# Kernel tuning notes

Measured on AMD Instinct MI355X. Metric: run time of the kernel, lower is better.

Reference implementation:

```python
import jax, jax.numpy as jnp
import numpy as np

EMBED_DIM = 768
NUM_HEADS = 12
HEAD_DIM = EMBED_DIM // NUM_HEADS

def setup_inputs() -> dict:
    key = jax.random.key(0)
    ks = jax.random.split(key, 5)
    B, N = 16, 1024
    s_qkv = 1.0 / np.sqrt(EMBED_DIM)
    s_proj = 1.0 / np.sqrt(EMBED_DIM)
    return {
        "x": jax.random.normal(ks[0], (B, N, EMBED_DIM), dtype=jnp.float32),
        "w_qkv": jax.random.uniform(ks[1], (EMBED_DIM, 3 * EMBED_DIM), jnp.float32, -s_qkv, s_qkv),
        "b_qkv": jax.random.uniform(ks[2], (3 * EMBED_DIM,), jnp.float32, -s_qkv, s_qkv),
        "w_proj": jax.random.uniform(ks[3], (EMBED_DIM, EMBED_DIM), jnp.float32, -s_proj, s_proj),
        "b_proj": jax.random.uniform(ks[4], (EMBED_DIM,), jnp.float32, -s_proj, s_proj),
    }

def reference(x, w_qkv, b_qkv, w_proj, b_proj):
    B, N, E = x.shape
    H, D = NUM_HEADS, HEAD_DIM
    qkv = x @ w_qkv + b_qkv                       # [B, N, 3E]
    qkv = qkv.reshape(B, N, 3, H, D)
    q, k, v = jnp.moveaxis(qkv, 2, 0)             # each [B, N, H, D]
    q = jnp.swapaxes(q, 1, 2)                      # [B, H, N, D]
    k = jnp.swapaxes(k, 1, 2)
    v = jnp.swapaxes(v, 1, 2)
    attn = jnp.einsum('bhnd,bhmd->bhnm', q, k) * (D ** -0.5)
    attn = jax.nn.softmax(attn, axis=-1)
    out = jnp.einsum('bhnm,bhmd->bhnd', attn, v)   # [B, H, N, D]
    out = jnp.swapaxes(out, 1, 2).reshape(B, N, E)
    return out @ w_proj + b_proj
```

## Files before the change

### kernel.cpp

```cpp
#include <hip/hip_runtime.h>
#include <hip/hip_bf16.h>


#define EDIM 768
#define NH 12
#define HD 64
#define BB 16
#define SN 1024
#define MTOT (BB*SN)

typedef __attribute__((ext_vector_type(8))) short short8;
typedef __attribute__((ext_vector_type(4))) short short4v;
typedef __attribute__((ext_vector_type(4))) float f32x4;
typedef unsigned short bfr;

#if defined(__HIP_DEVICE_COMPILE__)
#if !__has_builtin(__builtin_amdgcn_mfma_f32_16x16x16bf16_1k)
#error "missing __builtin_amdgcn_mfma_f32_16x16x16bf16_1k on device"
#endif
#endif

#define MFMA32(A,B,C) __builtin_amdgcn_mfma_f32_16x16x32_bf16(A,B,C,0,0,0)
#define MFMA16(A,B,C) __builtin_amdgcn_mfma_f32_16x16x16bf16_1k(A,B,C,0,0,0)

__device__ __forceinline__ bfr f2bf(float f) {
    union { float f; unsigned int u; } v; v.f = f;
    unsigned int u = v.u;
    u += 0x7FFFu + ((u >> 16) & 1u);
    return (bfr)(u >> 16);
}
__device__ __forceinline__ bfr f2bf_fast(float f) {
    union { float f; unsigned int u; } v; v.f = f;
    return (bfr)((v.u + 0x8000u) >> 16);
}

__device__ __forceinline__ void gl2lds16(const bfr* g, bfr* l) {
    __builtin_amdgcn_global_load_lds(
        (__attribute__((address_space(1))) void*)(g),
        (__attribute__((address_space(3))) void*)(l), 16, 0, 0);
}

__global__ void k_convert(const float* __restrict__ in, bfr* __restrict__ out, int n4) {
    const int j = (blockIdx.x & 7) * 1536 + (blockIdx.x >> 3);
    int i = j * blockDim.x + threadIdx.x;
    if (i >= n4) return;
    float4 v = ((const float4*)in)[i];
    ushort4 o;
    o.x = f2bf(v.x); o.y = f2bf(v.y); o.z = f2bf(v.z); o.w = f2bf(v.w);
    ((ushort4*)out)[i] = o;
}

__global__ void k_transpose_bf16(const float* __restrict__ in, bfr* __restrict__ out,
                                 int R, int C) {
    __shared__ float tile[32][33];
    int c0 = blockIdx.x * 32, r0 = blockIdx.y * 32;
    int tx = threadIdx.x & 31, ty = threadIdx.x >> 5;
    #pragma unroll
    for (int i = 0; i < 32; i += 8)
        tile[ty + i][tx] = in[(size_t)(r0 + ty + i) * C + c0 + tx];
    __syncthreads();
    #pragma unroll
    for (int i = 0; i < 32; i += 8)
        out[(size_t)(c0 + ty + i) * R + r0 + tx] = f2bf(tile[tx][ty + i]);
}

#define QSCALE 0.18033688011112042f
template <int EPI>
__launch_bounds__(256, 3)
__global__ void k_gemm_bt(const bfr* __restrict__ A, const bfr* __restrict__ BT,
                          const float* __restrict__ bias, float* __restrict__ out,
                          bfr* __restrict__ qb, bfr* __restrict__ kb, bfr* __restrict__ vT) {
    __shared__ bfr As[2][128 * 32];
    __shared__ bfr Bs[2][128 * 32];

    const int wgid = blockIdx.y * gridDim.x + blockIdx.x;
    const int xcd = wgid & 7;
    const int idx = wgid >> 3;
    const int half = gridDim.x << 3;
    const int band = idx / half;
    const int r = idx - band * half;
    const int n0 = (r >> 3) * 128;
    const int m0 = (xcd * 16 + band * 8 + (r & 7)) * 128;

    const int t = threadIdx.x;
    const int lane = t & 63;
    const int wave = t >> 6;
    const int wr = wave >> 1, wc = wave & 1;
    const int l15 = lane & 15, quad = lane >> 4;

    f32x4 acc[4][4] = {};

    const int srow = t >> 2;
    const int sg = ((t & 3) - (t >> 3)) & 3;
    const bfr* gA0 = A  + (size_t)(m0 + srow) * 768 + sg * 8;
    const bfr* gA1 = A  + (size_t)(m0 + 64 + srow) * 768 + sg * 8;
    const bfr* gB0 = BT + (size_t)(n0 + srow) * 768 + sg * 8;
    const bfr* gB1 = BT + (size_t)(n0 + 64 + srow) * 768 + sg * 8;
    const int w512 = wave * 512;

    const int pg = ((quad + (l15 >> 1)) & 3) * 8;

    for (int kt = 0; kt < 768; kt += 64) {
        __syncthreads();
        #pragma unroll
        for (int kh = 0; kh < 2; kh++) {
            const int ko = kt + kh * 32;
            gl2lds16(gA0 + ko, &As[kh][w512]);
            gl2lds16(gA1 + ko, &As[kh][2048 + w512]);
            gl2lds16(gB0 + ko, &Bs[kh][w512]);
            gl2lds16(gB1 + ko, &Bs[kh][2048 + w512]);
        }
        __syncthreads();

        #pragma unroll
        for (int kh = 0; kh < 2; kh++) {
            short8 af[4], bf[4];
            #pragma unroll
            for (int rt = 0; rt < 4; rt++)
                af[rt] = *(const short8*)(&As[kh][(wr * 64 + rt * 16 + l15) * 32 + pg]);
            #pragma unroll
            for (int ct = 0; ct < 4; ct++)
                bf[ct] = *(const short8*)(&Bs[kh][(wc * 64 + ct * 16 + l15) * 32 + pg]);
            #pragma unroll
            for (int rt = 0; rt < 4; rt++)
                #pragma unroll
                for (int ct = 0; ct < 4; ct++)
                    acc[rt][ct] = MFMA32(af[rt], bf[ct], acc[rt][ct]);
        }
    }

    #pragma unroll
    for (int rt = 0; rt < 4; rt++) {
        #pragma unroll
        for (int ct = 0; ct < 4; ct++) {
            const int col = n0 + wc * 64 + ct * 16 + l15;
            const float bv = bias[col];
            #pragma unroll
            for (int reg = 0; reg < 4; reg++) {
                const int m = m0 + wr * 64 + rt * 16 + quad * 4 + reg;
                float val = acc[rt][ct][reg] + bv;
                if constexpr (EPI == 0) {
                    out[(size_t)m * EDIM + col] = val;
                } else {
                    const int three = col / 768;
                    const int rem = col - three * 768;
                    const int h = rem >> 6, d = rem & 63;
                    const int b = m >> 10, n = m & 1023;
                    const size_t bh = (size_t)b * NH + h;
                    if (three == 0)      qb[(bh * SN + n) * HD + d] = f2bf(val * QSCALE);
                    else if (three == 1) kb[(bh * SN + n) * HD + d] = f2bf(val);
                    else                 vT[(bh * HD + d) * SN + n] = f2bf(val);
                }
            }
        }
    }
}

#define LDK 72

__launch_bounds__(256, 2)
__global__ void k_attn(const bfr* __restrict__ qb, const bfr* __restrict__ kb,
                       const bfr* __restrict__ vT, bfr* __restrict__ ao) {
    __shared__ bfr Ks[2][64 * LDK];
    __shared__ bfr Vs[2][64 * LDK];

    const int linear = blockIdx.y * gridDim.x + blockIdx.x;
    const int idx = linear >> 3;
    const int bh = (linear & 7) * 24 + idx % 24;
    const int q0 = (idx / 24) * 128;

    const int t = threadIdx.x;
    const int lane = t & 63, w = t >> 6;
    const int l15 = lane & 15, quad = lane >> 4;

    const bfr* qbase = qb + (size_t)bh * SN * HD;
    const bfr* kbase = kb + (size_t)bh * SN * HD;
    const bfr* vbase = vT + (size_t)bh * HD * SN;

    short8 qf[2][2];
    #pragma unroll
    for (int qt = 0; qt < 2; qt++)
        #pragma unroll
        for (int c = 0; c < 2; c++)
            qf[qt][c] = *(const short8*)(qbase + (size_t)(q0 + w * 32 + qt * 16 + l15) * HD + c * 32 + quad * 8);

    f32x4 o_acc[2][4] = {};
    f32x4 l_acc[2] = {};
    short4v ones4;
    #pragma unroll
    for (int i = 0; i < 4; i++) ones4[i] = (short)0x3F80;

    const int srow = t >> 2;
    const int scol = (t & 3) * 16;
    const bfr* gK = kbase + (size_t)srow * HD + scol;
    const bfr* gV = vbase + (size_t)srow * SN + scol;
    const int soff = srow * LDK + scol;

    uint4 kr0, kr1, vr0, vr1;
    kr0 = *(const uint4*)(gK);      kr1 = *(const uint4*)(gK + 8);
    vr0 = *(const uint4*)(gV);      vr1 = *(const uint4*)(gV + 8);
    *(uint4*)(&Ks[0][soff]) = kr0;  *(uint4*)(&Ks[0][soff + 8]) = kr1;
    *(uint4*)(&Vs[0][soff]) = vr0;  *(uint4*)(&Vs[0][soff + 8]) = vr1;

    for (int it = 0; it < SN / 64; it++) {
        const int cur = it & 1;
        const int kv0n = (it + 1) * 64;
        if (kv0n < SN) {
            kr0 = *(const uint4*)(gK + (size_t)kv0n * HD);
            kr1 = *(const uint4*)(gK + (size_t)kv0n * HD + 8);
            vr0 = *(const uint4*)(gV + kv0n);
            vr1 = *(const uint4*)(gV + kv0n + 8);
        }
        __syncthreads();
        if (kv0n < SN) {
            *(uint4*)(&Ks[cur ^ 1][soff]) = kr0;  *(uint4*)(&Ks[cur ^ 1][soff + 8]) = kr1;
            *(uint4*)(&Vs[cur ^ 1][soff]) = vr0;  *(uint4*)(&Vs[cur ^ 1][soff + 8]) = vr1;
        }

        const bfr* Kc = &Ks[cur][0];
        const bfr* Vc = &Vs[cur][0];

        short8 kf[4][2];
        #pragma unroll
        for (int kvt = 0; kvt < 4; kvt++)
            #pragma unroll
            for (int c = 0; c < 2; c++)
                kf[kvt][c] = *(const short8*)(Kc + (kvt * 16 + l15) * LDK + c * 32 + quad * 8);
        short4v vf[4][4];
        #pragma unroll
        for (int kvt = 0; kvt < 4; kvt++)
            #pragma unroll
            for (int ct = 0; ct < 4; ct++)
                vf[kvt][ct] = *(const short4v*)(Vc + (ct * 16 + l15) * LDK + kvt * 16 + quad * 4);

        f32x4 st[4][2] = {};
        #pragma unroll
        for (int c = 0; c < 2; c++)
            #pragma unroll
            for (int kvt = 0; kvt < 4; kvt++)
                #pragma unroll
                for (int qt = 0; qt < 2; qt++)
                    st[kvt][qt] = MFMA32(kf[kvt][c], qf[qt][c], st[kvt][qt]);

        short4v pf[4][2];
        #pragma unroll
        for (int kvt = 0; kvt < 4; kvt++)
            #pragma unroll
            for (int qt = 0; qt < 2; qt++) {
                union { unsigned u[2]; short4v s; } cv;
                cv.u[0] = (unsigned)f2bf_fast(exp2f(st[kvt][qt][0]))
                        | ((unsigned)f2bf_fast(exp2f(st[kvt][qt][1])) << 16);
                cv.u[1] = (unsigned)f2bf_fast(exp2f(st[kvt][qt][2]))
                        | ((unsigned)f2bf_fast(exp2f(st[kvt][qt][3])) << 16);
                pf[kvt][qt] = cv.s;
            }

        #pragma unroll
        for (int kvt = 0; kvt < 4; kvt++)
            #pragma unroll
            for (int qt = 0; qt < 2; qt++)
                l_acc[qt] = MFMA16(pf[kvt][qt], ones4, l_acc[qt]);
        #pragma unroll
        for (int kvt = 0; kvt < 4; kvt++)
            #pragma unroll
            for (int qt = 0; qt < 2; qt++)
                #pragma unroll
                for (int ct = 0; ct < 4; ct++)
                    o_acc[qt][ct] = MFMA16(pf[kvt][qt], vf[kvt][ct], o_acc[qt][ct]);
    }

    const int bb = bh / NH, h = bh % NH;
    #pragma unroll
    for (int qt = 0; qt < 2; qt++) {
        #pragma unroll
        for (int r = 0; r < 4; r++) {
            const float inv = 1.0f / l_acc[qt][r];
            const int n = q0 + w * 32 + qt * 16 + quad * 4 + r;
            #pragma unroll
            for (int ct = 0; ct < 4; ct++) {
                const int d = ct * 16 + l15;
                ao[((size_t)bb * SN + n) * EDIM + h * HD + d] = f2bf_fast(o_acc[qt][ct][r] * inv);
            }
        }
    }
}

extern "C" void kernel_launch(void* const* d_in, const int* in_sizes, int n_in,
                              void* d_out, int out_size, void* d_ws, size_t ws_size,
                              hipStream_t stream) {
    const float* x      = (const float*)d_in[0];
    const float* w_qkv  = (const float*)d_in[1];
    const float* b_qkv  = (const float*)d_in[2];
    const float* w_proj = (const float*)d_in[3];
    const float* b_proj = (const float*)d_in[4];

    char* ws = (char*)d_ws;
    bfr* xb     = (bfr*)(ws + 0);
    bfr* wqkvT  = (bfr*)(ws + 25165824);
    bfr* wprojT = (bfr*)(ws + 28704768);
    bfr* qb     = (bfr*)(ws + 29884416);
    bfr* kb     = (bfr*)(ws + 55050240);
    bfr* vT     = (bfr*)(ws + 80216064);
    bfr* ao     = (bfr*)(ws + 105381888);

    k_convert<<<12288, 256, 0, stream>>>(x, xb, (MTOT * EDIM) / 4);
    k_transpose_bf16<<<dim3(2304 / 32, 768 / 32), 256, 0, stream>>>(w_qkv, wqkvT, 768, 2304);
    k_transpose_bf16<<<dim3(768 / 32, 768 / 32), 256, 0, stream>>>(w_proj, wprojT, 768, 768);
    k_gemm_bt<1><<<dim3(2304 / 128, MTOT / 128), 256, 0, stream>>>(
        xb, wqkvT, b_qkv, nullptr, qb, kb, vT);
    k_attn<<<dim3(BB * NH, SN / 128), 256, 0, stream>>>(qb, kb, vT, ao);
    k_gemm_bt<0><<<dim3(768 / 128, MTOT / 128), 256, 0, stream>>>(
        ao, wprojT, b_proj, (float*)d_out, nullptr, nullptr, nullptr);
}
```

Before: 312.4 us.

## Stage V-transpose epilogue through LDS and read V directly from global in attention

In the QKV GEMM, blocks producing V columns now write their bias-added bf16 tile into shared memory transposed, then emit coalesced 16-byte stores into the vT layout instead of scattered 2-byte stores. Q/K epilogue is simplified to two branches. In the attention kernel, V is no longer staged through LDS; each wave loads its V fragments straight from global memory per iteration, which frees LDS and removes V stores and LDS reads, but relies on cache hits and adds global load latency inside the loop without double buffering.

```diff
diff --git a/kernel.cpp b/kernel.cpp
--- a/kernel.cpp
+++ b/kernel.cpp
@@ -65,20 +65,23 @@
 }
 
 #define QSCALE 0.18033688011112042f
+#define PST 136
+
 template <int EPI>
 __launch_bounds__(256, 3)
 __global__ void k_gemm_bt(const bfr* __restrict__ A, const bfr* __restrict__ BT,
                           const float* __restrict__ bias, float* __restrict__ out,
                           bfr* __restrict__ qb, bfr* __restrict__ kb, bfr* __restrict__ vT) {
-    __shared__ bfr As[2][128 * 32];
-    __shared__ bfr Bs[2][128 * 32];
+    __shared__ bfr smem[17408];
+    bfr* Asm = smem;
+    bfr* Bsm = smem + 8192;
 
     const int wgid = blockIdx.y * gridDim.x + blockIdx.x;
     const int xcd = wgid & 7;
     const int idx = wgid >> 3;
-    const int half = gridDim.x << 3;
-    const int band = idx / half;
-    const int r = idx - band * half;
+    const int half8 = gridDim.x << 3;
+    const int band = idx / half8;
+    const int r = idx - band * half8;
     const int n0 = (r >> 3) * 128;
     const int m0 = (xcd * 16 + band * 8 + (r & 7)) * 128;
 
@@ -105,10 +108,10 @@
         #pragma unroll
         for (int kh = 0; kh < 2; kh++) {
             const int ko = kt + kh * 32;
-            gl2lds16(gA0 + ko, &As[kh][w512]);
-            gl2lds16(gA1 + ko, &As[kh][2048 + w512]);
-            gl2lds16(gB0 + ko, &Bs[kh][w512]);
-            gl2lds16(gB1 + ko, &Bs[kh][2048 + w512]);
+            gl2lds16(gA0 + ko, &Asm[kh * 4096 + w512]);
+            gl2lds16(gA1 + ko, &Asm[kh * 4096 + 2048 + w512]);
+            gl2lds16(gB0 + ko, &Bsm[kh * 4096 + w512]);
+            gl2lds16(gB1 + ko, &Bsm[kh * 4096 + 2048 + w512]);
         }
         __syncthreads();
 
@@ -117,10 +120,10 @@
             short8 af[4], bf[4];
             #pragma unroll
             for (int rt = 0; rt < 4; rt++)
-                af[rt] = *(const short8*)(&As[kh][(wr * 64 + rt * 16 + l15) * 32 + pg]);
+                af[rt] = *(const short8*)(&Asm[kh * 4096 + (wr * 64 + rt * 16 + l15) * 32 + pg]);
             #pragma unroll
             for (int ct = 0; ct < 4; ct++)
-                bf[ct] = *(const short8*)(&Bs[kh][(wc * 64 + ct * 16 + l15) * 32 + pg]);
+                bf[ct] = *(const short8*)(&Bsm[kh * 4096 + (wc * 64 + ct * 16 + l15) * 32 + pg]);
             #pragma unroll
             for (int rt = 0; rt < 4; rt++)
                 #pragma unroll
@@ -129,30 +132,63 @@
         }
     }
 
-    #pragma unroll
-    for (int rt = 0; rt < 4; rt++) {
-        #pragma unroll
-        for (int ct = 0; ct < 4; ct++) {
-            const int col = n0 + wc * 64 + ct * 16 + l15;
-            const float bv = bias[col];
-            #pragma unroll
-            for (int reg = 0; reg < 4; reg++) {
-                const int m = m0 + wr * 64 + rt * 16 + quad * 4 + reg;
-                float val = acc[rt][ct][reg] + bv;
-                if constexpr (EPI == 0) {
-                    out[(size_t)m * EDIM + col] = val;
-                } else {
-                    const int three = col / 768;
-                    const int rem = col - three * 768;
-                    const int h = rem >> 6, d = rem & 63;
+    if constexpr (EPI == 0) {
+        #pragma unroll
+        for (int rt = 0; rt < 4; rt++)
+            #pragma unroll
+            for (int ct = 0; ct < 4; ct++) {
+                const int col = n0 + wc * 64 + ct * 16 + l15;
+                const float bv = bias[col];
+                #pragma unroll
+                for (int reg = 0; reg < 4; reg++) {
+                    const int m = m0 + wr * 64 + rt * 16 + quad * 4 + reg;
+                    out[(size_t)m * EDIM + col] = acc[rt][ct][reg] + bv;
+                }
+            }
+    } else if (n0 >= 1536) {
+        __syncthreads();
+        #pragma unroll
+        for (int rt = 0; rt < 4; rt++)
+            #pragma unroll
+            for (int ct = 0; ct < 4; ct++) {
+                const int cl = wc * 64 + ct * 16 + l15;
+                const float bv = bias[n0 + cl];
+                #pragma unroll
+                for (int reg = 0; reg < 4; reg++) {
+                    const int ml = wr * 64 + rt * 16 + quad * 4 + reg;
+                    smem[cl * PST + ml] = f2bf(acc[rt][ct][reg] + bv);
+                }
+            }
+        __syncthreads();
+        const int rr = t >> 1, hf = t & 1;
+        const int rem = n0 + rr - 1536;
+        const int h = rem >> 6, d = rem & 63;
+        const int b = m0 >> 10, nb = m0 & 1023;
+        bfr* dst = vT + ((size_t)(b * NH + h) * HD + d) * SN + nb + hf * 64;
+        const bfr* src = smem + rr * PST + hf * 64;
+        #pragma unroll
+        for (int i = 0; i < 8; i++)
+            *(uint4*)(dst + i * 8) = *(const uint4*)(src + i * 8);
+    } else {
+        #pragma unroll
+        for (int rt = 0; rt < 4; rt++)
+            #pragma unroll
+            for (int ct = 0; ct < 4; ct++) {
+                const int col = n0 + wc * 64 + ct * 16 + l15;
+                const float bv = bias[col];
+                const int isq = (col < 768);
+                const int rem = col - (isq ? 0 : 768);
+                const int h = rem >> 6, d = rem & 63;
+                #pragma unroll
+                for (int reg = 0; reg < 4; reg++) {
+                    const int m = m0 + wr * 64 + rt * 16 + quad * 4 + reg;
                     const int b = m >> 10, n = m & 1023;
                     const size_t bh = (size_t)b * NH + h;
-                    if (three == 0)      qb[(bh * SN + n) * HD + d] = f2bf(val * QSCALE);
-                    else if (three == 1) kb[(bh * SN + n) * HD + d] = f2bf(val);
-                    else                 vT[(bh * HD + d) * SN + n] = f2bf(val);
+                    float val = acc[rt][ct][reg] + bv;
+                    if (isq) qb[(bh * SN + n) * HD + d] = f2bf(val * QSCALE);
+                    else     kb[(bh * SN + n) * HD + d] = f2bf(val);
                 }
             }
-        }
     }
 }
 
@@ -162,7 +198,6 @@
 __global__ void k_attn(const bfr* __restrict__ qb, const bfr* __restrict__ kb,
                        const bfr* __restrict__ vT, bfr* __restrict__ ao) {
     __shared__ bfr Ks[2][64 * LDK];
-    __shared__ bfr Vs[2][64 * LDK];
 
     const int linear = blockIdx.y * gridDim.x + blockIdx.x;
     const int idx = linear >> 3;
@@ -193,45 +228,42 @@
     const int srow = t >> 2;
     const int scol = (t & 3) * 16;
     const bfr* gK = kbase + (size_t)srow * HD + scol;
-    const bfr* gV = vbase + (size_t)srow * SN + scol;
     const int soff = srow * LDK + scol;
 
-    uint4 kr0, kr1, vr0, vr1;
+    uint4 kr0, kr1;
     kr0 = *(const uint4*)(gK);      kr1 = *(const uint4*)(gK + 8);
-    vr0 = *(const uint4*)(gV);      vr1 = *(const uint4*)(gV + 8);
     *(uint4*)(&Ks[0][soff]) = kr0;  *(uint4*)(&Ks[0][soff + 8]) = kr1;
-    *(uint4*)(&Vs[0][soff]) = vr0;  *(uint4*)(&Vs[0][soff + 8]) = vr1;
 
     for (int it = 0; it < SN / 64; it++) {
         const int cur = it & 1;
-        const int kv0n = (it + 1) * 64;
+        const int kv0 = it * 64;
+        const int kv0n = kv0 + 64;
+
+        short4v vf[4][4];
+        #pragma unroll
+        for (int kvt = 0; kvt < 4; kvt++)
+            #pragma unroll
+            for (int ct = 0; ct < 4; ct++)
+                vf[kvt][ct] = *(const short4v*)(vbase + (size_t)(ct * 16 + l15) * SN
+                                                + kv0 + kvt * 16 + quad * 4);
+
         if (kv0n < SN) {
             kr0 = *(const uint4*)(gK + (size_t)kv0n * HD);
             kr1 = *(const uint4*)(gK + (size_t)kv0n * HD + 8);
-            vr0 = *(const uint4*)(gV + kv0n);
-            vr1 = *(const uint4*)(gV + kv0n + 8);
         }
         __syncthreads();
         if (kv0n < SN) {
-            *(uint4*)(&Ks[cur ^ 1][soff]) = kr0;  *(uint4*)(&Ks[cur ^ 1][soff + 8]) = kr1;
-            *(uint4*)(&Vs[cur ^ 1][soff]) = vr0;  *(uint4*)(&Vs[cur ^ 1][soff + 8]) = vr1;
+            *(uint4*)(&Ks[cur ^ 1][soff]) = kr0;
+            *(uint4*)(&Ks[cur ^ 1][soff + 8]) = kr1;
         }
 
         const bfr* Kc = &Ks[cur][0];
-        const bfr* Vc = &Vs[cur][0];
-
         short8 kf[4][2];
         #pragma unroll
         for (int kvt = 0; kvt < 4; kvt++)
             #pragma unroll
             for (int c = 0; c < 2; c++)
                 kf[kvt][c] = *(const short8*)(Kc + (kvt * 16 + l15) * LDK + c * 32 + quad * 8);
-        short4v vf[4][4];
-        #pragma unroll
-        for (int kvt = 0; kvt < 4; kvt++)
-            #pragma unroll
-            for (int ct = 0; ct < 4; ct++)
-                vf[kvt][ct] = *(const short4v*)(Vc + (ct * 16 + l15) * LDK + kvt * 16 + quad * 4);
 
         f32x4 st[4][2] = {};
         #pragma unroll
```

New measurement: 393.5 us. +26.0%, slower.
